# Kernel tuning notes

Hardware: AMD Instinct MI355X
Metric: run time of the kernel (lower is better)

The kernel has to match this reference:

```python
import jax, jax.numpy as jnp
import numpy as np

TEMPERATURE = 11.313708498984761  # sqrt(128)


def setup_inputs() -> dict:
    key = jax.random.key(0)
    kq, kk, kv = jax.random.split(key, 3)
    b, n, m, d, dv = 16, 2048, 2048, 128, 128
    return {
        "queries": jax.random.normal(kq, (b, n, d), dtype=jnp.float32),
        "keys": jax.random.normal(kk, (b, m, d), dtype=jnp.float32),
        "values": jax.random.normal(kv, (b, m, dv), dtype=jnp.float32),
    }


def reference(queries, keys, values):
    # scores: [b, n, m]
    scores = jnp.einsum('bnd,bmd->bnm', queries, keys) / TEMPERATURE
    attn = jax.nn.softmax(scores, axis=2)
    # out: [b, n, d']
    return jnp.einsum('bnm,bmd->bnd', attn, values)
```

## Files before the change

kernel.cpp:

```cpp
#include <hip/hip_runtime.h>
#include <hip/hip_bf16.h>


#define BATCH 16
#define SEQ   2048
#define DIM   128

typedef short bf16x8 __attribute__((ext_vector_type(8)));
typedef float f32x16 __attribute__((ext_vector_type(16)));

static __device__ inline unsigned pk2(float lo, float hi) {
  union { float f; unsigned u; } a, b;
  a.f = lo; b.f = hi;
  return ((b.u + 0x8000u) & 0xffff0000u) | ((a.u + 0x8000u) >> 16);
}
static __device__ inline unsigned short f2bf(float f) {
  union { float f; unsigned u; } v; v.f = f;
  return (unsigned short)((v.u + 0x8000u) >> 16);
}
static __device__ inline float fast_exp2(float x) {
#if __has_builtin(__builtin_amdgcn_exp2f)
  return __builtin_amdgcn_exp2f(x);
#else
  return exp2f(x);
#endif
}

__global__ __launch_bounds__(256)
void prep_kernel(const float* __restrict__ K, const float* __restrict__ V,
                 unsigned short* __restrict__ Kb, unsigned short* __restrict__ Vt,
                 float scale) {
  const int bx = blockIdx.x, tid = threadIdx.x;
  if (bx < 2048) {
    size_t idx = (size_t)bx * 256 + tid;
    const float4* kf = (const float4*)K;
    float4 a = kf[idx * 2], c = kf[idx * 2 + 1];
    uint4 o;
    o.x = pk2(a.x * scale, a.y * scale);
    o.y = pk2(a.z * scale, a.w * scale);
    o.z = pk2(c.x * scale, c.y * scale);
    o.w = pk2(c.z * scale, c.w * scale);
    ((uint4*)Kb)[idx] = o;
  } else {
    __shared__ float tile[128][33];
    const int vb = bx - 2048;
    const int b = vb >> 6, r = vb & 63;
    const int m0 = (r & 15) * 128, d0 = (r >> 4) * 32;
    const int c = tid & 7, mr = tid >> 3;
    const float* src = V + ((size_t)(b * SEQ) + m0) * DIM + d0;
#pragma unroll
    for (int it = 0; it < 4; ++it) {
      int m = it * 32 + mr;
      float4 x = *(const float4*)(src + (size_t)m * DIM + c * 4);
      tile[m][c * 4 + 0] = x.x; tile[m][c * 4 + 1] = x.y;
      tile[m][c * 4 + 2] = x.z; tile[m][c * 4 + 3] = x.w;
    }
    __syncthreads();
    const int dr = tid >> 3, s = tid & 7;
    unsigned short* dst = Vt + ((size_t)(b * DIM) + d0 + dr) * SEQ + m0;
#pragma unroll
    for (int it = 0; it < 2; ++it) {
      int slot = it * 8 + s;
      uint4 o;
      o.x = pk2(tile[slot * 8 + 0][dr], tile[slot * 8 + 1][dr]);
      o.y = pk2(tile[slot * 8 + 2][dr], tile[slot * 8 + 3][dr]);
      o.z = pk2(tile[slot * 8 + 4][dr], tile[slot * 8 + 5][dr]);
      o.w = pk2(tile[slot * 8 + 6][dr], tile[slot * 8 + 7][dr]);
      *(uint4*)(dst + slot * 8) = o;
    }
  }
}

#define KS_OFF 0
#define VS_OFF 8704
#define PS_OFF 17920

__global__ __launch_bounds__(256, 2)
void attn_kernel(const float* __restrict__ Qf,
                 const unsigned short* __restrict__ Kb,
                 const unsigned short* __restrict__ Vtb,
                 float* __restrict__ out) {
  __shared__ __align__(16) unsigned short smem[22528];

  const int tid  = threadIdx.x;
  const int wv   = tid >> 6;
  const int w_q  = wv & 1;
  const int w_m  = wv >> 1;
  const int lane = tid & 63;
  const int l31  = lane & 31;
  const int q2   = lane >> 5;
  const int b    = blockIdx.x;
  const int q0   = blockIdx.y * 64 + w_q * 32;

  bf16x8 aq[8];
  {
    const float* qp = Qf + ((size_t)(b * SEQ) + q0 + l31) * DIM + q2 * 8;
#pragma unroll
    for (int c = 0; c < 8; ++c) {
      float4 x = *(const float4*)(qp + c * 16);
      float4 y = *(const float4*)(qp + c * 16 + 4);
      union { unsigned i[4]; bf16x8 v; } u;
      u.i[0] = pk2(x.x, x.y); u.i[1] = pk2(x.z, x.w);
      u.i[2] = pk2(y.x, y.y); u.i[3] = pk2(y.z, y.w);
      aq[c] = u.v;
    }
  }

  f32x16 oacc[4];
#pragma unroll
  for (int t = 0; t < 4; ++t)
#pragma unroll
    for (int i = 0; i < 16; ++i) oacc[t][i] = 0.0f;
  float lsum[16];
#pragma unroll
  for (int i = 0; i < 16; ++i) lsum[i] = 0.0f;

  const unsigned short* kb = Kb  + (size_t)b * SEQ * DIM;
  const unsigned short* vb = Vtb + (size_t)b * SEQ * DIM;
  unsigned short* ps = smem + PS_OFF + w_q * 2304;

  for (int kt = 0; kt < SEQ / 64; ++kt) {
    const int m0 = kt * 64;
    __syncthreads();
#pragma unroll
    for (int i = 0; i < 4; ++i) {
      int id = i * 256 + tid, row = id >> 4, c = id & 15;
      uint4 v = *(const uint4*)(kb + (size_t)(m0 + row) * DIM + c * 8);
      *(uint4*)(smem + KS_OFF + row * 136 + c * 8) = v;
    }
#pragma unroll
    for (int i = 0; i < 4; ++i) {
      int id = i * 256 + tid, dv = id >> 3, c = id & 7;
      uint4 v = *(const uint4*)(vb + (size_t)dv * SEQ + m0 + c * 8);
      *(uint4*)(smem + VS_OFF + dv * 72 + c * 8) = v;
    }
    __syncthreads();

    f32x16 s;
#pragma unroll
    for (int i = 0; i < 16; ++i) s[i] = 0.0f;
#pragma unroll
    for (int c = 0; c < 8; ++c) {
      bf16x8 bk = *(const bf16x8*)(smem + KS_OFF + (w_m * 32 + l31) * 136 + c * 16 + q2 * 8);
      s = __builtin_amdgcn_mfma_f32_32x32x16_bf16(aq[c], bk, s, 0, 0, 0);
    }

    float p[16];
#pragma unroll
    for (int i = 0; i < 16; ++i) { p[i] = fast_exp2(s[i]); lsum[i] += p[i]; }

#pragma unroll
    for (int r = 0; r < 16; ++r) {
      int qr = (r & 3) + ((r >> 2) << 3) + (q2 << 2);
      ps[qr * 72 + w_m * 32 + l31] = f2bf(p[r]);
    }
    asm volatile("s_waitcnt lgkmcnt(0)\n" ::: "memory");
    bf16x8 pf0 = *(const bf16x8*)(ps + l31 * 72 + w_m * 32 + q2 * 8);
    bf16x8 pf1 = *(const bf16x8*)(ps + l31 * 72 + w_m * 32 + 16 + q2 * 8);

#pragma unroll
    for (int t = 0; t < 4; ++t) {
      bf16x8 bv0 = *(const bf16x8*)(smem + VS_OFF + (t * 32 + l31) * 72 + w_m * 32 + q2 * 8);
      oacc[t] = __builtin_amdgcn_mfma_f32_32x32x16_bf16(pf0, bv0, oacc[t], 0, 0, 0);
      bf16x8 bv1 = *(const bf16x8*)(smem + VS_OFF + (t * 32 + l31) * 72 + w_m * 32 + 16 + q2 * 8);
      oacc[t] = __builtin_amdgcn_mfma_f32_32x32x16_bf16(pf1, bv1, oacc[t], 0, 0, 0);
    }
  }

#pragma unroll
  for (int r = 0; r < 16; ++r) {
    float v = lsum[r];
#pragma unroll
    for (int m = 1; m < 32; m <<= 1) v += __shfl_xor(v, m, 64);
    lsum[r] = v;
  }

  __syncthreads();
  float* cb  = (float*)smem;
  float* cbL = cb + 8192;
  if (w_m == 1) {
    float* my = cb + w_q * 4096;
#pragma unroll
    for (int t = 0; t < 4; ++t)
#pragma unroll
      for (int r = 0; r < 16; ++r)
        my[(t * 16 + r) * 64 + lane] = oacc[t][r];
    if (l31 == 0) {
#pragma unroll
      for (int r = 0; r < 16; ++r) {
        int qr = (r & 3) + ((r >> 2) << 3) + (q2 << 2);
        cbL[w_q * 32 + qr] = lsum[r];
      }
    }
  }
  __syncthreads();
  if (w_m == 0) {
    const float* pr = cb + w_q * 4096;
    float linv[16];
#pragma unroll
    for (int r = 0; r < 16; ++r) {
      int qr = (r & 3) + ((r >> 2) << 3) + (q2 << 2);
      linv[r] = 1.0f / (lsum[r] + cbL[w_q * 32 + qr]);
    }
    float* ob = out + ((size_t)(b * SEQ) + q0) * DIM;
#pragma unroll
    for (int t = 0; t < 4; ++t)
#pragma unroll
      for (int r = 0; r < 16; ++r) {
        int qr = (r & 3) + ((r >> 2) << 3) + (q2 << 2);
        ob[(size_t)qr * DIM + t * 32 + l31] = (oacc[t][r] + pr[(t * 16 + r) * 64 + lane]) * linv[r];
      }
  }
}

extern "C" void kernel_launch(void* const* d_in, const int* in_sizes, int n_in,
                              void* d_out, int out_size, void* d_ws, size_t ws_size,
                              hipStream_t stream) {
  const float* Q = (const float*)d_in[0];
  const float* K = (const float*)d_in[1];
  const float* V = (const float*)d_in[2];
  float* out = (float*)d_out;

  const size_t elems = (size_t)BATCH * SEQ * DIM;
  unsigned short* Kb = (unsigned short*)d_ws;
  unsigned short* Vt = Kb + elems;

  const double TEMPERATURE = 11.313708498984761;
  const float scale = (float)(1.4426950408889634 / TEMPERATURE);

  prep_kernel<<<3072, 256, 0, stream>>>(K, V, Kb, Vt, scale);
  attn_kernel<<<dim3(BATCH, SEQ / 64), 256, 0, stream>>>(Q, Kb, Vt, out);
}
```

Baseline: 143.6 us.

## Enlarge attention tiles, register-prefetch K/V, swizzle LDS, shuffle P without LDS

The attention kernel now uses 512-thread blocks covering 128 queries and 128-key tiles. Each wave computes two 32-query score tiles from one K fragment, so each LDS K/V read is reused across more queries. The next K/V tile is prefetched into registers while the current tile's MFMAs run, and LDS uses an XOR swizzle in place of padding. Probabilities are packed and exchanged through cross-lane shuffles rather than written to and re-read from LDS. The epilogue reduces the four key-split partial outputs serially through LDS, which adds syncs, and the larger register footprint may limit occupancy.

Result: slower. 255.4 us (+77.8%).

```diff
diff --git a/kernel.cpp b/kernel.cpp
--- a/kernel.cpp
+++ b/kernel.cpp
@@ -5,6 +5,7 @@
 #define BATCH 16
 #define SEQ   2048
 #define DIM   128
+#define NT    (SEQ / 128)
 
 typedef short bf16x8 __attribute__((ext_vector_type(8)));
 typedef float f32x16 __attribute__((ext_vector_type(16)));
@@ -13,10 +14,6 @@
   union { float f; unsigned u; } a, b;
   a.f = lo; b.f = hi;
   return ((b.u + 0x8000u) & 0xffff0000u) | ((a.u + 0x8000u) >> 16);
-}
-static __device__ inline unsigned short f2bf(float f) {
-  union { float f; unsigned u; } v; v.f = f;
-  return (unsigned short)((v.u + 0x8000u) >> 16);
 }
 static __device__ inline float fast_exp2(float x) {
 #if __has_builtin(__builtin_amdgcn_exp2f)
@@ -71,30 +68,58 @@
   }
 }
 
-#define KS_OFF 0
-#define VS_OFF 8704
-#define PS_OFF 17920
-
-__global__ __launch_bounds__(256, 2)
+#define SWZ(row, c) (((row) << 8) + ((((c) ^ ((row) & 7))) << 4))
+
+static __device__ inline void tile_p(const f32x16& s, int q2, float& lsum,
+                                     bf16x8& f0o, bf16x8& f1o) {
+  float p[16];
+#pragma unroll
+  for (int i = 0; i < 16; ++i) p[i] = fast_exp2(s[i]);
+  lsum += (((p[0]+p[1])+(p[2]+p[3])) + ((p[4]+p[5])+(p[6]+p[7])))
+        + (((p[8]+p[9])+(p[10]+p[11])) + ((p[12]+p[13])+(p[14]+p[15])));
+  unsigned d0 = pk2(p[0],  p[1]),  d1 = pk2(p[2],  p[3]);
+  unsigned d2 = pk2(p[4],  p[5]),  d3 = pk2(p[6],  p[7]);
+  unsigned d4 = pk2(p[8],  p[9]),  d5 = pk2(p[10], p[11]);
+  unsigned d6 = pk2(p[12], p[13]), d7 = pk2(p[14], p[15]);
+  unsigned t0 = (unsigned)__shfl_xor((int)(q2 ? d0 : d2), 32, 64);
+  unsigned t1 = (unsigned)__shfl_xor((int)(q2 ? d1 : d3), 32, 64);
+  unsigned t2 = (unsigned)__shfl_xor((int)(q2 ? d4 : d6), 32, 64);
+  unsigned t3 = (unsigned)__shfl_xor((int)(q2 ? d5 : d7), 32, 64);
+  union { unsigned i[4]; bf16x8 v; } f0, f1;
+  f0.i[0] = q2 ? t0 : d0;  f0.i[1] = q2 ? t1 : d1;
+  f0.i[2] = q2 ? d2 : t0;  f0.i[3] = q2 ? d3 : t1;
+  f1.i[0] = q2 ? t2 : d4;  f1.i[1] = q2 ? t3 : d5;
+  f1.i[2] = q2 ? d6 : t2;  f1.i[3] = q2 ? d7 : t3;
+  f0o = f0.v; f1o = f1.v;
+}
+
+__global__ __launch_bounds__(512, 2)
 void attn_kernel(const float* __restrict__ Qf,
                  const unsigned short* __restrict__ Kb,
                  const unsigned short* __restrict__ Vtb,
                  float* __restrict__ out) {
-  __shared__ __align__(16) unsigned short smem[22528];
+  __shared__ __align__(16) char smem[65536];
+  char* Ks = smem;
+  char* Vs = smem + 32768;
 
   const int tid  = threadIdx.x;
-  const int wv   = tid >> 6;
-  const int w_q  = wv & 1;
-  const int w_m  = wv >> 1;
+  const int wave = tid >> 6;
+  const int w_q  = wave & 1;
+  const int w_m  = wave >> 1;
   const int lane = tid & 63;
   const int l31  = lane & 31;
   const int q2   = lane >> 5;
   const int b    = blockIdx.x;
-  const int q0   = blockIdx.y * 64 + w_q * 32;
-
-  bf16x8 aq[8];
-  {
-    const float* qp = Qf + ((size_t)(b * SEQ) + q0 + l31) * DIM + q2 * 8;
+  const int by   = blockIdx.y;
+  const int mch  = w_m * 32;
+
+  const unsigned short* kb = Kb  + (size_t)b * SEQ * DIM;
+  const unsigned short* vb = Vtb + (size_t)b * SEQ * DIM;
+
+  bf16x8 bq[2][8];
+#pragma unroll
+  for (int qt = 0; qt < 2; ++qt) {
+    const float* qp = Qf + ((size_t)(b * SEQ) + by * 128 + w_q * 64 + qt * 32 + l31) * DIM + q2 * 8;
 #pragma unroll
     for (int c = 0; c < 8; ++c) {
       float4 x = *(const float4*)(qp + c * 16);
@@ -102,114 +127,115 @@
       union { unsigned i[4]; bf16x8 v; } u;
       u.i[0] = pk2(x.x, x.y); u.i[1] = pk2(x.z, x.w);
       u.i[2] = pk2(y.x, y.y); u.i[3] = pk2(y.z, y.w);
-      aq[c] = u.v;
-    }
-  }
-
-  f32x16 oacc[4];
-#pragma unroll
-  for (int t = 0; t < 4; ++t)
-#pragma unroll
-    for (int i = 0; i < 16; ++i) oacc[t][i] = 0.0f;
-  float lsum[16];
-#pragma unroll
-  for (int i = 0; i < 16; ++i) lsum[i] = 0.0f;
-
-  const unsigned short* kb = Kb  + (size_t)b * SEQ * DIM;
-  const unsigned short* vb = Vtb + (size_t)b * SEQ * DIM;
-  unsigned short* ps = smem + PS_OFF + w_q * 2304;
-
-  for (int kt = 0; kt < SEQ / 64; ++kt) {
-    const int m0 = kt * 64;
+      bq[qt][c] = u.v;
+    }
+  }
+
+  uint4 kr[4], vr[4];
+#pragma unroll
+  for (int i = 0; i < 4; ++i) {
+    int id = i * 512 + tid, row = id >> 4, c = id & 15;
+    kr[i] = *(const uint4*)(kb + (size_t)row * DIM + c * 8);
+    vr[i] = *(const uint4*)(vb + (size_t)row * SEQ + c * 8);
+  }
+
+  f32x16 oacc[4][2];
+#pragma unroll
+  for (int dvt = 0; dvt < 4; ++dvt)
+#pragma unroll
+    for (int qt = 0; qt < 2; ++qt)
+#pragma unroll
+      for (int i = 0; i < 16; ++i) oacc[dvt][qt][i] = 0.0f;
+  float lsum[2] = {0.0f, 0.0f};
+
+  for (int kt = 0; kt < NT; ++kt) {
     __syncthreads();
 #pragma unroll
     for (int i = 0; i < 4; ++i) {
-      int id = i * 256 + tid, row = id >> 4, c = id & 15;
-      uint4 v = *(const uint4*)(kb + (size_t)(m0 + row) * DIM + c * 8);
-      *(uint4*)(smem + KS_OFF + row * 136 + c * 8) = v;
-    }
-#pragma unroll
-    for (int i = 0; i < 4; ++i) {
-      int id = i * 256 + tid, dv = id >> 3, c = id & 7;
-      uint4 v = *(const uint4*)(vb + (size_t)dv * SEQ + m0 + c * 8);
-      *(uint4*)(smem + VS_OFF + dv * 72 + c * 8) = v;
-    }
-    __syncthreads();
-
-    f32x16 s;
-#pragma unroll
-    for (int i = 0; i < 16; ++i) s[i] = 0.0f;
+      int id = i * 512 + tid, row = id >> 4, c = id & 15;
+      *(uint4*)(Ks + SWZ(row, c)) = kr[i];
+      *(uint4*)(Vs + SWZ(row, c)) = vr[i];
+    }
+    __syncthreads();
+
+    f32x16 s0, s1;
+#pragma unroll
+    for (int i = 0; i < 16; ++i) { s0[i] = 0.0f; s1[i] = 0.0f; }
 #pragma unroll
     for (int c = 0; c < 8; ++c) {
-      bf16x8 bk = *(const bf16x8*)(smem + KS_OFF + (w_m * 32 + l31) * 136 + c * 16 + q2 * 8);
-      s = __builtin_amdgcn_mfma_f32_32x32x16_bf16(aq[c], bk, s, 0, 0, 0);
-    }
-
-    float p[16];
-#pragma unroll
-    for (int i = 0; i < 16; ++i) { p[i] = fast_exp2(s[i]); lsum[i] += p[i]; }
-
-#pragma unroll
-    for (int r = 0; r < 16; ++r) {
-      int qr = (r & 3) + ((r >> 2) << 3) + (q2 << 2);
-      ps[qr * 72 + w_m * 32 + l31] = f2bf(p[r]);
-    }
-    asm volatile("s_waitcnt lgkmcnt(0)\n" ::: "memory");
-    bf16x8 pf0 = *(const bf16x8*)(ps + l31 * 72 + w_m * 32 + q2 * 8);
-    bf16x8 pf1 = *(const bf16x8*)(ps + l31 * 72 + w_m * 32 + 16 + q2 * 8);
-
-#pragma unroll
-    for (int t = 0; t < 4; ++t) {
-      bf16x8 bv0 = *(const bf16x8*)(smem + VS_OFF + (t * 32 + l31) * 72 + w_m * 32 + q2 * 8);
-      oacc[t] = __builtin_amdgcn_mfma_f32_32x32x16_bf16(pf0, bv0, oacc[t], 0, 0, 0);
-      bf16x8 bv1 = *(const bf16x8*)(smem + VS_OFF + (t * 32 + l31) * 72 + w_m * 32 + 16 + q2 * 8);
-      oacc[t] = __builtin_amdgcn_mfma_f32_32x32x16_bf16(pf1, bv1, oacc[t], 0, 0, 0);
-    }
-  }
-
-#pragma unroll
-  for (int r = 0; r < 16; ++r) {
-    float v = lsum[r];
-#pragma unroll
-    for (int m = 1; m < 32; m <<= 1) v += __shfl_xor(v, m, 64);
-    lsum[r] = v;
-  }
+      bf16x8 ak = *(const bf16x8*)(Ks + SWZ(mch + l31, c * 2 + q2));
+      s0 = __builtin_amdgcn_mfma_f32_32x32x16_bf16(ak, bq[0][c], s0, 0, 0, 0);
+      s1 = __builtin_amdgcn_mfma_f32_32x32x16_bf16(ak, bq[1][c], s1, 0, 0, 0);
+    }
+
+    if (kt + 1 < NT) {
+      const int m0 = (kt + 1) * 128;
+#pragma unroll
+      for (int i = 0; i < 4; ++i) {
+        int id = i * 512 + tid, row = id >> 4, c = id & 15;
+        kr[i] = *(const uint4*)(kb + (size_t)(m0 + row) * DIM + c * 8);
+        vr[i] = *(const uint4*)(vb + (size_t)row * SEQ + m0 + c * 8);
+      }
+    }
+
+    bf16x8 pf00, pf01, pf10, pf11;
+    tile_p(s0, q2, lsum[0], pf00, pf01);
+    tile_p(s1, q2, lsum[1], pf10, pf11);
+
+#pragma unroll
+    for (int dvt = 0; dvt < 4; ++dvt) {
+      bf16x8 av0 = *(const bf16x8*)(Vs + SWZ(dvt * 32 + l31, w_m * 4 + q2));
+      bf16x8 av1 = *(const bf16x8*)(Vs + SWZ(dvt * 32 + l31, w_m * 4 + 2 + q2));
+      oacc[dvt][0] = __builtin_amdgcn_mfma_f32_32x32x16_bf16(av0, pf00, oacc[dvt][0], 0, 0, 0);
+      oacc[dvt][0] = __builtin_amdgcn_mfma_f32_32x32x16_bf16(av1, pf01, oacc[dvt][0], 0, 0, 0);
+      oacc[dvt][1] = __builtin_amdgcn_mfma_f32_32x32x16_bf16(av0, pf10, oacc[dvt][1], 0, 0, 0);
+      oacc[dvt][1] = __builtin_amdgcn_mfma_f32_32x32x16_bf16(av1, pf11, oacc[dvt][1], 0, 0, 0);
+    }
+  }
+
+  lsum[0] += __shfl_xor(lsum[0], 32, 64);
+  lsum[1] += __shfl_xor(lsum[1], 32, 64);
 
   __syncthreads();
-  float* cb  = (float*)smem;
-  float* cbL = cb + 8192;
-  if (w_m == 1) {
-    float* my = cb + w_q * 4096;
-#pragma unroll
-    for (int t = 0; t < 4; ++t)
-#pragma unroll
-      for (int r = 0; r < 16; ++r)
-        my[(t * 16 + r) * 64 + lane] = oacc[t][r];
-    if (l31 == 0) {
-#pragma unroll
-      for (int r = 0; r < 16; ++r) {
-        int qr = (r & 3) + ((r >> 2) << 3) + (q2 << 2);
-        cbL[w_q * 32 + qr] = lsum[r];
+  float* Ob = (float*)smem;
+  float* Ls = (float*)(smem + 33024);
+
+  for (int half = 0; half < 2; ++half) {
+#pragma unroll
+    for (int ph = 0; ph < 4; ++ph) {
+      if (w_q == half && w_m == ph) {
+#pragma unroll
+        for (int qt = 0; qt < 2; ++qt) {
+#pragma unroll
+          for (int dvt = 0; dvt < 4; ++dvt) {
+#pragma unroll
+            for (int r = 0; r < 16; ++r) {
+              int q  = qt * 32 + l31;
+              int dv = dvt * 32 + (r & 3) + 8 * (r >> 2) + 4 * q2;
+              float v = oacc[dvt][qt][r];
+              if (ph) v += Ob[q * 129 + dv];
+              Ob[q * 129 + dv] = v;
+            }
+          }
+          if (q2 == 0) Ls[w_m * 64 + qt * 32 + l31] = lsum[qt];
+        }
       }
-    }
-  }
-  __syncthreads();
-  if (w_m == 0) {
-    const float* pr = cb + w_q * 4096;
-    float linv[16];
-#pragma unroll
-    for (int r = 0; r < 16; ++r) {
-      int qr = (r & 3) + ((r >> 2) << 3) + (q2 << 2);
-      linv[r] = 1.0f / (lsum[r] + cbL[w_q * 32 + qr]);
-    }
-    float* ob = out + ((size_t)(b * SEQ) + q0) * DIM;
-#pragma unroll
-    for (int t = 0; t < 4; ++t)
-#pragma unroll
-      for (int r = 0; r < 16; ++r) {
-        int qr = (r & 3) + ((r >> 2) << 3) + (q2 << 2);
-        ob[(size_t)qr * DIM + t * 32 + l31] = (oacc[t][r] + pr[(t * 16 + r) * 64 + lane]) * linv[r];
-      }
+      __syncthreads();
+    }
+    float* ob = out + ((size_t)(b * SEQ) + by * 128 + half * 64) * DIM;
+#pragma unroll
+    for (int j = 0; j < 4; ++j) {
+      int fid = j * 512 + tid;
+      int q = fid >> 5, dvi = fid & 31;
+      float linv = 1.0f / (Ls[q] + Ls[64 + q] + Ls[128 + q] + Ls[192 + q]);
+      float4 o;
+      o.x = Ob[q * 129 + dvi * 4 + 0] * linv;
+      o.y = Ob[q * 129 + dvi * 4 + 1] * linv;
+      o.z = Ob[q * 129 + dvi * 4 + 2] * linv;
+      o.w = Ob[q * 129 + dvi * 4 + 3] * linv;
+      *(float4*)(ob + (size_t)q * DIM + dvi * 4) = o;
+    }
+    __syncthreads();
   }
 }
 
@@ -229,5 +255,5 @@
   const float scale = (float)(1.4426950408889634 / TEMPERATURE);
 
   prep_kernel<<<3072, 256, 0, stream>>>(K, V, Kb, Vt, scale);
-  attn_kernel<<<dim3(BATCH, SEQ / 64), 256, 0, stream>>>(Q, Kb, Vt, out);
-}
+  attn_kernel<<<dim3(BATCH, SEQ / 128), 512, 0, stream>>>(Q, Kb, Vt, out);
+}
```
